# Optimization experiments

Hardware: AMD Instinct MI355X
Metric: run time of the kernel (lower is better)

The kernel has to match this reference:

```python
import jax, jax.numpy as jnp
import numpy as np

N_NODES = 100_000
N_FACES = 200_000
IN_CH = 128
OUT_CH = 29  # MLP out = OUT_CH + 3


def setup_inputs() -> dict:
    key = jax.random.key(0)
    k_pos, k_faces, k_ff, k_w1, k_w2 = jax.random.split(key, 5)
    pos = jax.random.normal(k_pos, (N_NODES, 3), dtype=jnp.float32)
    faces = jax.random.randint(k_faces, (N_FACES, 3), 0, N_NODES, dtype=jnp.int32)
    face_features = jax.random.normal(k_ff, (N_FACES, IN_CH), dtype=jnp.float32)
    d_in = IN_CH + 6
    W1 = jax.random.normal(k_w1, (d_in, IN_CH), dtype=jnp.float32) / np.sqrt(d_in)
    b1 = jnp.zeros((IN_CH,), dtype=jnp.float32)
    W2 = jax.random.normal(k_w2, (IN_CH, OUT_CH + 3), dtype=jnp.float32) / np.sqrt(IN_CH)
    b2 = jnp.zeros((OUT_CH + 3,), dtype=jnp.float32)
    return {"pos": pos, "face_features": face_features, "W1": W1, "b1": b1,
            "W2": W2, "b2": b2, "faces": faces}


def reference(pos, face_features, W1, b1, W2, b2, faces):
    def mlp(x):
        return jax.nn.relu(x @ W1 + b1) @ W2 + b2

    p0 = pos[faces[:, 0]]  # [F,3]
    p1 = pos[faces[:, 1]]
    p2 = pos[faces[:, 2]]

    g0 = mlp(jnp.concatenate([p1 - p0, p2 - p0, face_features], axis=1))
    g1 = mlp(jnp.concatenate([p2 - p1, p0 - p1, face_features], axis=1))
    g2 = mlp(jnp.concatenate([p0 - p2, p1 - p2, face_features], axis=1))

    face_features_out = (g0[:, 3:] + g1[:, 3:] + g2[:, 3:]) / 3.0  # [F,OUT_CH]

    # scatter_mean of per-corner deltas onto nodes; torch cat order matches
    # faces.T.flatten() = [faces[:,0], faces[:,1], faces[:,2]]
    vals = jnp.concatenate([g0[:, :3], g1[:, :3], g2[:, :3]], axis=0)  # [3F,3]
    idx = jnp.concatenate([faces[:, 0], faces[:, 1], faces[:, 2]], axis=0)  # [3F]
    sums = jax.ops.segment_sum(vals, idx, num_segments=N_NODES)
    counts = jax.ops.segment_sum(jnp.ones((vals.shape[0],), vals.dtype), idx,
                                 num_segments=N_NODES)
    delta_pos = sums / jnp.clip(counts, 1.0)[:, None]  # [N,3]

    new_pos = pos + delta_pos
    return (delta_pos, new_pos, face_features_out)
```

## Files before the change

### kernel.cpp

```cpp
#include <hip/hip_runtime.h>
#include <hip/hip_bf16.h>

#define N_NODES 100000
#define N_FACES 200000
#define FM 32
#define ROWS 96
#define XS 168
#define HS 136
#define WCS 40
#define W2S 136
#define NCH 5

typedef __attribute__((ext_vector_type(8))) short s8v;
typedef __attribute__((ext_vector_type(4))) short s4v;
typedef __attribute__((ext_vector_type(4))) float f4v;

static __device__ __forceinline__ short f2bf(float x) {
  __hip_bfloat16 h = __float2bfloat16(x);
  short s;
  __builtin_memcpy(&s, &h, 2);
  return s;
}

__global__ __launch_bounds__(256) void prep_kernel(
    const float* __restrict__ W1, const float* __restrict__ W2,
    short* __restrict__ w1t, short* __restrict__ w2t)
{
  int t = blockIdx.x * 256 + threadIdx.x;
  if (t < NCH * 128 * WCS) {
    int kc = t / (128 * WCS);
    int r = t % (128 * WCS);
    int n = r / WCS, kk = r % WCS;
    float v = 0.f;
    if (kk < 32) {
      int k = kc * 32 + kk;
      int gk = (k < 128) ? (k + 6) : (k < 134 ? k - 128 : -1);
      if (gk >= 0) v = W1[gk * 128 + n];
    }
    w1t[t] = f2bf(v);
  }
  if (t < 32 * W2S) {
    int o = t / W2S, k = t % W2S;
    float v = (k < 128) ? W2[k * 32 + o] : 0.f;
    w2t[t] = f2bf(v);
  }
}

__global__ __launch_bounds__(256) void face_kernel(
    const float* __restrict__ pos, const float* __restrict__ ffeat,
    const float* __restrict__ b1, const float* __restrict__ b2,
    const int* __restrict__ faces,
    const short* __restrict__ w1t_g, const short* __restrict__ w2t_g,
    float* __restrict__ out_ff, float* __restrict__ sums, int* __restrict__ cnt)
{
  __shared__ short xh[ROWS * XS];
  __shared__ short wb[2][128 * WCS];
  __shared__ short w2[32 * W2S];

  const int t = threadIdx.x;
  const int lane = t & 63;
  const int wv = t >> 6;
  const int l15 = lane & 15;
  const int lq = lane >> 4;
  const int kq = lq * 8;
  const int fbase = blockIdx.x * FM;

  {
    const unsigned* src = (const unsigned*)w2t_g;
    unsigned* dst = (unsigned*)w2;
#pragma unroll
    for (int i = 0; i < 9; ++i) {
      int idx = i * 256 + t;
      if (idx < (32 * W2S) / 2) dst[idx] = src[idx];
    }
  }
#pragma unroll
  for (int i = 0; i < 4; ++i) {
    int e = i * 256 + t;
    int floc = e >> 5, c4 = e & 31;
    f4v v = *(const f4v*)(ffeat + ((size_t)(fbase + floc) << 7) + (c4 << 2));
    s4v s;
    s.x = f2bf(v.x); s.y = f2bf(v.y); s.z = f2bf(v.z); s.w = f2bf(v.w);
    *(s4v*)&xh[(0 * FM + floc) * XS + (c4 << 2)] = s;
    *(s4v*)&xh[(1 * FM + floc) * XS + (c4 << 2)] = s;
    *(s4v*)&xh[(2 * FM + floc) * XS + (c4 << 2)] = s;
  }
  if (t < ROWS) {
    int v = t >> 5, floc = t & 31, face = fbase + floc;
    int vb = (v == 2) ? 0 : v + 1;
    int vc = (v == 0) ? 2 : v - 1;
    int ia = faces[face * 3 + v];
    int ib = faces[face * 3 + vb];
    int ic = faces[face * 3 + vc];
    float ax = pos[ia * 3 + 0], ay = pos[ia * 3 + 1], az = pos[ia * 3 + 2];
    float bx = pos[ib * 3 + 0], by = pos[ib * 3 + 1], bz = pos[ib * 3 + 2];
    float cx = pos[ic * 3 + 0], cy = pos[ic * 3 + 1], cz = pos[ic * 3 + 2];
    short* xr = &xh[t * XS];
    xr[128] = f2bf(bx - ax); xr[129] = f2bf(by - ay); xr[130] = f2bf(bz - az);
    xr[131] = f2bf(cx - ax); xr[132] = f2bf(cy - ay); xr[133] = f2bf(cz - az);
#pragma unroll
    for (int c = 134; c < XS; ++c) xr[c] = 0;
  }
  const unsigned* w1u = (const unsigned*)w1t_g;
  {
    unsigned* dst = (unsigned*)wb[0];
#pragma unroll
    for (int i = 0; i < 10; ++i) dst[i * 256 + t] = w1u[i * 256 + t];
  }
  __syncthreads();

  f4v acc[6][2];
#pragma unroll
  for (int m = 0; m < 6; ++m)
#pragma unroll
    for (int n = 0; n < 2; ++n) acc[m][n] = (f4v){0.f, 0.f, 0.f, 0.f};

#pragma unroll
  for (int kc = 0; kc < NCH; ++kc) {
    if (kc + 1 < NCH) {
      unsigned* dst = (unsigned*)wb[(kc + 1) & 1];
      const unsigned* src = w1u + (kc + 1) * (128 * WCS / 2);
#pragma unroll
      for (int i = 0; i < 10; ++i) dst[i * 256 + t] = src[i * 256 + t];
    }
    const short* wc = wb[kc & 1];
    s8v bf0 = *(const s8v*)&wc[((wv * 2 + 0) * 16 + l15) * WCS + kq];
    s8v bf1 = *(const s8v*)&wc[((wv * 2 + 1) * 16 + l15) * WCS + kq];
#pragma unroll
    for (int m = 0; m < 6; ++m) {
      s8v af = *(const s8v*)&xh[(m * 16 + l15) * XS + kc * 32 + kq];
      acc[m][0] = __builtin_amdgcn_mfma_f32_16x16x32_bf16(af, bf0, acc[m][0], 0, 0, 0);
      acc[m][1] = __builtin_amdgcn_mfma_f32_16x16x32_bf16(af, bf1, acc[m][1], 0, 0, 0);
    }
    __syncthreads();
  }

#pragma unroll
  for (int n = 0; n < 2; ++n) {
    int j = (wv * 2 + n) * 16 + l15;
    float bj = b1[j];
#pragma unroll
    for (int m = 0; m < 6; ++m) {
      int rb = m * 16 + lq * 4;
#pragma unroll
      for (int r = 0; r < 4; ++r) {
        float h = acc[m][n][r] + bj;
        xh[(rb + r) * HS + j] = f2bf(fmaxf(h, 0.f));
      }
    }
  }
  __syncthreads();

  f4v a2[3];
#pragma unroll
  for (int c = 0; c < 3; ++c) a2[c] = (f4v){0.f, 0.f, 0.f, 0.f};
  const int ct0 = wv * 3;
#pragma unroll
  for (int kk = 0; kk < 4; ++kk) {
    int kof = kk * 32 + kq;
#pragma unroll
    for (int c = 0; c < 3; ++c) {
      int ct = ct0 + c, mt = ct >> 1, n = ct & 1;
      s8v a = *(const s8v*)&xh[(mt * 16 + l15) * HS + kof];
      s8v b = *(const s8v*)&w2[(n * 16 + l15) * W2S + kof];
      a2[c] = __builtin_amdgcn_mfma_f32_16x16x32_bf16(a, b, a2[c], 0, 0, 0);
    }
  }
  __syncthreads();

  float* gsum = (float*)xh;
#pragma unroll
  for (int c = 0; c < 3; ++c) {
    int ct = ct0 + c, mt = ct >> 1, n = ct & 1;
    int o = n * 16 + l15;
    float bo = b2[o];
#pragma unroll
    for (int r = 0; r < 4; ++r) {
      int row = mt * 16 + lq * 4 + r;
      float g = a2[c][r] + bo;
      if (o < 3) {
        int v = row >> 5, floc = row & 31;
        int node = faces[(fbase + floc) * 3 + v];
        atomicAdd(&sums[node * 3 + o], g);
        if (o == 0) atomicAdd(&cnt[node], 1);
      } else {
        gsum[row * 29 + (o - 3)] = g;
      }
    }
  }
  __syncthreads();

#pragma unroll
  for (int i = 0; i < 4; ++i) {
    int e = i * 256 + t;
    if (e < FM * 29) {
      int floc = e / 29, c = e % 29;
      float s = gsum[floc * 29 + c] + gsum[(FM + floc) * 29 + c] + gsum[(2 * FM + floc) * 29 + c];
      out_ff[(size_t)(fbase + floc) * 29 + c] = s * (1.0f / 3.0f);
    }
  }
}

__global__ __launch_bounds__(256) void node_kernel(
    const float* __restrict__ pos, const float* __restrict__ sums,
    const int* __restrict__ cnt, float* __restrict__ out)
{
  int n = blockIdx.x * 256 + threadIdx.x;
  if (n >= N_NODES) return;
  float c = fmaxf((float)cnt[n], 1.0f);
#pragma unroll
  for (int o = 0; o < 3; ++o) {
    float d = sums[n * 3 + o] / c;
    out[n * 3 + o] = d;
    out[3 * N_NODES + n * 3 + o] = pos[n * 3 + o] + d;
  }
}

extern "C" void kernel_launch(void* const* d_in, const int* in_sizes, int n_in,
                              void* d_out, int out_size, void* d_ws, size_t ws_size,
                              hipStream_t stream) {
  const float* pos   = (const float*)d_in[0];
  const float* ffeat = (const float*)d_in[1];
  const float* W1    = (const float*)d_in[2];
  const float* b1    = (const float*)d_in[3];
  const float* W2    = (const float*)d_in[4];
  const float* b2    = (const float*)d_in[5];
  const int*   faces = (const int*)d_in[6];
  float* out = (float*)d_out;

  float* sums = (float*)d_ws;
  int*   cnt  = (int*)(sums + 3 * N_NODES);
  short* w1t  = (short*)(cnt + N_NODES);
  short* w2t  = w1t + NCH * 128 * WCS;

  hipMemsetAsync(d_ws, 0, (size_t)(3 * N_NODES + N_NODES) * 4, stream);
  prep_kernel<<<100, 256, 0, stream>>>(W1, W2, w1t, w2t);
  face_kernel<<<N_FACES / FM, 256, 0, stream>>>(pos, ffeat, b1, b2, faces, w1t, w2t,
                                                out + 6 * N_NODES, sums, cnt);
  node_kernel<<<(N_NODES + 255) / 256, 256, 0, stream>>>(pos, sums, cnt, out);
}
```

Before: 296.2 us.

## Make face kernel persistent with register-resident weights and double-buffered tile prefetch

The face kernel becomes a persistent grid of 512 blocks of 512 threads, each looping over many 32-face tiles. W1 and W2 fragments are held in registers, loaded once per block, instead of being streamed through shared memory for every tile. Face features, face indices and edge vectors for the next tile are prefetched into double-buffered shared memory while the current tile's MFMAs run. Features are stored once, not three times, and the per-corner outputs are summed with LDS atomics. The cost is more registers per thread, lower occupancy, and some repeated MFMAs on identical feature fragments.

```diff
diff --git a/kernel.cpp b/kernel.cpp
--- a/kernel.cpp
+++ b/kernel.cpp
@@ -5,11 +5,13 @@
 #define N_FACES 200000
 #define FM 32
 #define ROWS 96
-#define XS 168
+#define NTILES (N_FACES / FM)
+#define GRID 512
+#define FS 136
+#define ES 40
 #define HS 136
-#define WCS 40
-#define W2S 136
-#define NCH 5
+#define W1K 160
+#define W2K 128
 
 typedef __attribute__((ext_vector_type(8))) short s8v;
 typedef __attribute__((ext_vector_type(4))) short s4v;
@@ -27,35 +29,31 @@
     short* __restrict__ w1t, short* __restrict__ w2t)
 {
   int t = blockIdx.x * 256 + threadIdx.x;
-  if (t < NCH * 128 * WCS) {
-    int kc = t / (128 * WCS);
-    int r = t % (128 * WCS);
-    int n = r / WCS, kk = r % WCS;
+  if (t < 128 * W1K) {
+    int n = t / W1K, k = t % W1K;
     float v = 0.f;
-    if (kk < 32) {
-      int k = kc * 32 + kk;
-      int gk = (k < 128) ? (k + 6) : (k < 134 ? k - 128 : -1);
-      if (gk >= 0) v = W1[gk * 128 + n];
-    }
+    if (k < 128) v = W1[(k + 6) * 128 + n];
+    else if (k < 134) v = W1[(k - 128) * 128 + n];
     w1t[t] = f2bf(v);
   }
-  if (t < 32 * W2S) {
-    int o = t / W2S, k = t % W2S;
-    float v = (k < 128) ? W2[k * 32 + o] : 0.f;
-    w2t[t] = f2bf(v);
-  }
-}
-
-__global__ __launch_bounds__(256) void face_kernel(
+  if (t < 32 * W2K) {
+    int o = t / W2K, k = t % W2K;
+    w2t[t] = f2bf(W2[k * 32 + o]);
+  }
+}
+
+__global__ __launch_bounds__(512, 4) void face_kernel(
     const float* __restrict__ pos, const float* __restrict__ ffeat,
     const float* __restrict__ b1, const float* __restrict__ b2,
     const int* __restrict__ faces,
     const short* __restrict__ w1t_g, const short* __restrict__ w2t_g,
     float* __restrict__ out_ff, float* __restrict__ sums, int* __restrict__ cnt)
 {
-  __shared__ short xh[ROWS * XS];
-  __shared__ short wb[2][128 * WCS];
-  __shared__ short w2[32 * W2S];
+  __shared__ short xff[2][FM * FS];
+  __shared__ short xe[2][ROWS * ES];
+  __shared__ short hbuf[ROWS * HS];
+  __shared__ int   nidb[2][ROWS];
+  __shared__ float gsumb[FM * 30];
 
   const int t = threadIdx.x;
   const int lane = t & 63;
@@ -63,140 +61,172 @@
   const int l15 = lane & 15;
   const int lq = lane >> 4;
   const int kq = lq * 8;
-  const int fbase = blockIdx.x * FM;
+  const int nsel = wv & 1;
+
+  s8v bw1[5], bw2[4];
+#pragma unroll
+  for (int kc = 0; kc < 5; ++kc)
+    bw1[kc] = *(const s8v*)(w1t_g + (wv * 16 + l15) * W1K + kc * 32 + kq);
+#pragma unroll
+  for (int kk = 0; kk < 4; ++kk)
+    bw2[kk] = *(const s8v*)(w2t_g + (nsel * 16 + l15) * W2K + kk * 32 + kq);
+  const float b1j = b1[wv * 16 + l15];
+  const float b2o = b2[nsel * 16 + l15];
+
+  if (t < 2 * ROWS) {
+    int b = t / ROWS, row = t - b * ROWS;
+    s8v z = (s8v){0, 0, 0, 0, 0, 0, 0, 0};
+    *(unsigned*)&xe[b][row * ES + 6] = 0u;
+    *(s8v*)&xe[b][row * ES + 8] = z;
+    *(s8v*)&xe[b][row * ES + 16] = z;
+    *(s8v*)&xe[b][row * ES + 24] = z;
+    *(s8v*)&xe[b][row * ES + 32] = z;
+  }
 
   {
-    const unsigned* src = (const unsigned*)w2t_g;
-    unsigned* dst = (unsigned*)w2;
-#pragma unroll
-    for (int i = 0; i < 9; ++i) {
-      int idx = i * 256 + t;
-      if (idx < (32 * W2S) / 2) dst[idx] = src[idx];
-    }
-  }
-#pragma unroll
-  for (int i = 0; i < 4; ++i) {
-    int e = i * 256 + t;
-    int floc = e >> 5, c4 = e & 31;
-    f4v v = *(const f4v*)(ffeat + ((size_t)(fbase + floc) << 7) + (c4 << 2));
-    s4v s;
-    s.x = f2bf(v.x); s.y = f2bf(v.y); s.z = f2bf(v.z); s.w = f2bf(v.w);
-    *(s4v*)&xh[(0 * FM + floc) * XS + (c4 << 2)] = s;
-    *(s4v*)&xh[(1 * FM + floc) * XS + (c4 << 2)] = s;
-    *(s4v*)&xh[(2 * FM + floc) * XS + (c4 << 2)] = s;
-  }
-  if (t < ROWS) {
-    int v = t >> 5, floc = t & 31, face = fbase + floc;
-    int vb = (v == 2) ? 0 : v + 1;
-    int vc = (v == 0) ? 2 : v - 1;
-    int ia = faces[face * 3 + v];
-    int ib = faces[face * 3 + vb];
-    int ic = faces[face * 3 + vc];
-    float ax = pos[ia * 3 + 0], ay = pos[ia * 3 + 1], az = pos[ia * 3 + 2];
-    float bx = pos[ib * 3 + 0], by = pos[ib * 3 + 1], bz = pos[ib * 3 + 2];
-    float cx = pos[ic * 3 + 0], cy = pos[ic * 3 + 1], cz = pos[ic * 3 + 2];
-    short* xr = &xh[t * XS];
-    xr[128] = f2bf(bx - ax); xr[129] = f2bf(by - ay); xr[130] = f2bf(bz - az);
-    xr[131] = f2bf(cx - ax); xr[132] = f2bf(cy - ay); xr[133] = f2bf(cz - az);
-#pragma unroll
-    for (int c = 134; c < XS; ++c) xr[c] = 0;
-  }
-  const unsigned* w1u = (const unsigned*)w1t_g;
-  {
-    unsigned* dst = (unsigned*)wb[0];
-#pragma unroll
-    for (int i = 0; i < 10; ++i) dst[i * 256 + t] = w1u[i * 256 + t];
+    int fb = blockIdx.x * FM;
+    const float* fp = ffeat + ((size_t)(fb + (t >> 4)) << 7) + ((t & 15) << 3);
+    f4v v0 = *(const f4v*)fp, v1 = *(const f4v*)(fp + 4);
+    s8v s;
+    s[0] = f2bf(v0.x); s[1] = f2bf(v0.y); s[2] = f2bf(v0.z); s[3] = f2bf(v0.w);
+    s[4] = f2bf(v1.x); s[5] = f2bf(v1.y); s[6] = f2bf(v1.z); s[7] = f2bf(v1.w);
+    *(s8v*)&xff[0][(t >> 4) * FS + ((t & 15) << 3)] = s;
+    int rt = t - 384;
+    if ((unsigned)rt < 96u) {
+      int face = fb + (rt & 31), v = rt >> 5;
+      int i0 = faces[face * 3 + 0], i1 = faces[face * 3 + 1], i2 = faces[face * 3 + 2];
+      int ia = (v == 0) ? i0 : ((v == 1) ? i1 : i2);
+      int ib = (v == 0) ? i1 : ((v == 1) ? i2 : i0);
+      int ic = (v == 0) ? i2 : ((v == 1) ? i0 : i1);
+      float ax = pos[ia * 3], ay = pos[ia * 3 + 1], az = pos[ia * 3 + 2];
+      float bx = pos[ib * 3], by = pos[ib * 3 + 1], bz = pos[ib * 3 + 2];
+      float cx = pos[ic * 3], cy = pos[ic * 3 + 1], cz = pos[ic * 3 + 2];
+      s4v e;
+      e[0] = f2bf(bx - ax); e[1] = f2bf(by - ay); e[2] = f2bf(bz - az); e[3] = f2bf(cx - ax);
+      *(s4v*)&xe[0][rt * ES] = e;
+      unsigned p2 = (unsigned)(unsigned short)f2bf(cy - ay) |
+                    ((unsigned)(unsigned short)f2bf(cz - az) << 16);
+      *(unsigned*)&xe[0][rt * ES + 4] = p2;
+      nidb[0][rt] = ia;
+    }
   }
   __syncthreads();
 
-  f4v acc[6][2];
-#pragma unroll
-  for (int m = 0; m < 6; ++m)
-#pragma unroll
-    for (int n = 0; n < 2; ++n) acc[m][n] = (f4v){0.f, 0.f, 0.f, 0.f};
-
-#pragma unroll
-  for (int kc = 0; kc < NCH; ++kc) {
-    if (kc + 1 < NCH) {
-      unsigned* dst = (unsigned*)wb[(kc + 1) & 1];
-      const unsigned* src = w1u + (kc + 1) * (128 * WCS / 2);
-#pragma unroll
-      for (int i = 0; i < 10; ++i) dst[i * 256 + t] = src[i * 256 + t];
-    }
-    const short* wc = wb[kc & 1];
-    s8v bf0 = *(const s8v*)&wc[((wv * 2 + 0) * 16 + l15) * WCS + kq];
-    s8v bf1 = *(const s8v*)&wc[((wv * 2 + 1) * 16 + l15) * WCS + kq];
+  int iter = 0;
+  for (int tile = blockIdx.x; tile < NTILES; tile += GRID, ++iter) {
+    const int cur = iter & 1, nxt = cur ^ 1;
+    const int fb_c = tile * FM;
+    const int tile_n = tile + GRID;
+    const bool hn = tile_n < NTILES;
+    const int fb_n = tile_n * FM;
+    const int rt = t - 384;
+
+    f4v nv0, nv1;
+    int ni0 = 0, ni1 = 0, ni2 = 0;
+    if (hn) {
+      const float* fp = ffeat + ((size_t)(fb_n + (t >> 4)) << 7) + ((t & 15) << 3);
+      nv0 = *(const f4v*)fp;
+      nv1 = *(const f4v*)(fp + 4);
+      if ((unsigned)rt < 96u) {
+        int face = fb_n + (rt & 31);
+        ni0 = faces[face * 3 + 0]; ni1 = faces[face * 3 + 1]; ni2 = faces[face * 3 + 2];
+      }
+    }
+
+    f4v acc1[6];
+#pragma unroll
+    for (int m = 0; m < 6; ++m) acc1[m] = (f4v){0.f, 0.f, 0.f, 0.f};
+    const short* xf = &xff[cur][0];
+    const short* xeb = &xe[cur][0];
+#pragma unroll
+    for (int kc = 0; kc < 4; ++kc) {
+      s8v a0 = *(const s8v*)&xf[l15 * FS + kc * 32 + kq];
+      s8v a1 = *(const s8v*)&xf[(16 + l15) * FS + kc * 32 + kq];
+      acc1[0] = __builtin_amdgcn_mfma_f32_16x16x32_bf16(a0, bw1[kc], acc1[0], 0, 0, 0);
+      acc1[1] = __builtin_amdgcn_mfma_f32_16x16x32_bf16(a1, bw1[kc], acc1[1], 0, 0, 0);
+      acc1[2] = __builtin_amdgcn_mfma_f32_16x16x32_bf16(a0, bw1[kc], acc1[2], 0, 0, 0);
+      acc1[3] = __builtin_amdgcn_mfma_f32_16x16x32_bf16(a1, bw1[kc], acc1[3], 0, 0, 0);
+      acc1[4] = __builtin_amdgcn_mfma_f32_16x16x32_bf16(a0, bw1[kc], acc1[4], 0, 0, 0);
+      acc1[5] = __builtin_amdgcn_mfma_f32_16x16x32_bf16(a1, bw1[kc], acc1[5], 0, 0, 0);
+    }
 #pragma unroll
     for (int m = 0; m < 6; ++m) {
-      s8v af = *(const s8v*)&xh[(m * 16 + l15) * XS + kc * 32 + kq];
-      acc[m][0] = __builtin_amdgcn_mfma_f32_16x16x32_bf16(af, bf0, acc[m][0], 0, 0, 0);
-      acc[m][1] = __builtin_amdgcn_mfma_f32_16x16x32_bf16(af, bf1, acc[m][1], 0, 0, 0);
-    }
+      s8v a = *(const s8v*)&xeb[(m * 16 + l15) * ES + kq];
+      acc1[m] = __builtin_amdgcn_mfma_f32_16x16x32_bf16(a, bw1[4], acc1[m], 0, 0, 0);
+    }
+
     __syncthreads();
-  }
-
-#pragma unroll
-  for (int n = 0; n < 2; ++n) {
-    int j = (wv * 2 + n) * 16 + l15;
-    float bj = b1[j];
-#pragma unroll
-    for (int m = 0; m < 6; ++m) {
-      int rb = m * 16 + lq * 4;
-#pragma unroll
-      for (int r = 0; r < 4; ++r) {
-        float h = acc[m][n][r] + bj;
-        xh[(rb + r) * HS + j] = f2bf(fmaxf(h, 0.f));
+
+    {
+      int j = wv * 16 + l15;
+#pragma unroll
+      for (int m = 0; m < 6; ++m)
+#pragma unroll
+        for (int r = 0; r < 4; ++r)
+          hbuf[(m * 16 + lq * 4 + r) * HS + j] = f2bf(fmaxf(acc1[m][r] + b1j, 0.f));
+    }
+    for (int e = t; e < FM * 30; e += 512) gsumb[e] = 0.f;
+
+    float pax = 0, pay = 0, paz = 0, pbx = 0, pby = 0, pbz = 0, pcx = 0, pcy = 0, pcz = 0;
+    int ia_s = 0, ib_s = 0, ic_s = 0;
+    if (hn) {
+      s8v s;
+      s[0] = f2bf(nv0.x); s[1] = f2bf(nv0.y); s[2] = f2bf(nv0.z); s[3] = f2bf(nv0.w);
+      s[4] = f2bf(nv1.x); s[5] = f2bf(nv1.y); s[6] = f2bf(nv1.z); s[7] = f2bf(nv1.w);
+      *(s8v*)&xff[nxt][(t >> 4) * FS + ((t & 15) << 3)] = s;
+      if ((unsigned)rt < 96u) {
+        int v = rt >> 5;
+        ia_s = (v == 0) ? ni0 : ((v == 1) ? ni1 : ni2);
+        ib_s = (v == 0) ? ni1 : ((v == 1) ? ni2 : ni0);
+        ic_s = (v == 0) ? ni2 : ((v == 1) ? ni0 : ni1);
+        pax = pos[ia_s * 3]; pay = pos[ia_s * 3 + 1]; paz = pos[ia_s * 3 + 2];
+        pbx = pos[ib_s * 3]; pby = pos[ib_s * 3 + 1]; pbz = pos[ib_s * 3 + 2];
+        pcx = pos[ic_s * 3]; pcy = pos[ic_s * 3 + 1]; pcz = pos[ic_s * 3 + 2];
       }
     }
-  }
-  __syncthreads();
-
-  f4v a2[3];
-#pragma unroll
-  for (int c = 0; c < 3; ++c) a2[c] = (f4v){0.f, 0.f, 0.f, 0.f};
-  const int ct0 = wv * 3;
-#pragma unroll
-  for (int kk = 0; kk < 4; ++kk) {
-    int kof = kk * 32 + kq;
-#pragma unroll
-    for (int c = 0; c < 3; ++c) {
-      int ct = ct0 + c, mt = ct >> 1, n = ct & 1;
-      s8v a = *(const s8v*)&xh[(mt * 16 + l15) * HS + kof];
-      s8v b = *(const s8v*)&w2[(n * 16 + l15) * W2S + kof];
-      a2[c] = __builtin_amdgcn_mfma_f32_16x16x32_bf16(a, b, a2[c], 0, 0, 0);
-    }
-  }
-  __syncthreads();
-
-  float* gsum = (float*)xh;
-#pragma unroll
-  for (int c = 0; c < 3; ++c) {
-    int ct = ct0 + c, mt = ct >> 1, n = ct & 1;
-    int o = n * 16 + l15;
-    float bo = b2[o];
-#pragma unroll
-    for (int r = 0; r < 4; ++r) {
-      int row = mt * 16 + lq * 4 + r;
-      float g = a2[c][r] + bo;
-      if (o < 3) {
-        int v = row >> 5, floc = row & 31;
-        int node = faces[(fbase + floc) * 3 + v];
-        atomicAdd(&sums[node * 3 + o], g);
-        if (o == 0) atomicAdd(&cnt[node], 1);
-      } else {
-        gsum[row * 29 + (o - 3)] = g;
+    __syncthreads();
+
+#pragma unroll
+    for (int p = 0; p < 2; ++p) {
+      if (p == 0 || wv < 4) {
+        int m = (wv >> 1) + p * 4;
+        f4v c2 = (f4v){0.f, 0.f, 0.f, 0.f};
+#pragma unroll
+        for (int kk = 0; kk < 4; ++kk) {
+          s8v a = *(const s8v*)&hbuf[(m * 16 + l15) * HS + kk * 32 + kq];
+          c2 = __builtin_amdgcn_mfma_f32_16x16x32_bf16(a, bw2[kk], c2, 0, 0, 0);
+        }
+        int o = nsel * 16 + l15;
+#pragma unroll
+        for (int r = 0; r < 4; ++r) {
+          int row = m * 16 + lq * 4 + r;
+          float g = c2[r] + b2o;
+          if (o < 3) {
+            int node = nidb[cur][row];
+            atomicAdd(&sums[node * 3 + o], g);
+            if (o == 0) atomicAdd(&cnt[node], 1);
+          } else {
+            atomicAdd(&gsumb[(row & 31) * 30 + (o - 3)], g);
+          }
+        }
       }
     }
-  }
-  __syncthreads();
-
-#pragma unroll
-  for (int i = 0; i < 4; ++i) {
-    int e = i * 256 + t;
-    if (e < FM * 29) {
-      int floc = e / 29, c = e % 29;
-      float s = gsum[floc * 29 + c] + gsum[(FM + floc) * 29 + c] + gsum[(2 * FM + floc) * 29 + c];
-      out_ff[(size_t)(fbase + floc) * 29 + c] = s * (1.0f / 3.0f);
+
+    if (hn && (unsigned)rt < 96u) {
+      s4v e;
+      e[0] = f2bf(pbx - pax); e[1] = f2bf(pby - pay);
+      e[2] = f2bf(pbz - paz); e[3] = f2bf(pcx - pax);
+      *(s4v*)&xe[nxt][rt * ES] = e;
+      unsigned p2 = (unsigned)(unsigned short)f2bf(pcy - pay) |
+                    ((unsigned)(unsigned short)f2bf(pcz - paz) << 16);
+      *(unsigned*)&xe[nxt][rt * ES + 4] = p2;
+      nidb[nxt][rt] = ia_s;
+    }
+    __syncthreads();
+
+    for (int e = t; e < FM * 29; e += 512) {
+      int floc = e / 29, c = e - floc * 29;
+      out_ff[((size_t)(fb_c + floc)) * 29 + c] = gsumb[floc * 30 + c] * (1.0f / 3.0f);
     }
   }
 }
@@ -231,11 +261,11 @@
   float* sums = (float*)d_ws;
   int*   cnt  = (int*)(sums + 3 * N_NODES);
   short* w1t  = (short*)(cnt + N_NODES);
-  short* w2t  = w1t + NCH * 128 * WCS;
+  short* w2t  = w1t + 128 * W1K;
 
   hipMemsetAsync(d_ws, 0, (size_t)(3 * N_NODES + N_NODES) * 4, stream);
-  prep_kernel<<<100, 256, 0, stream>>>(W1, W2, w1t, w2t);
-  face_kernel<<<N_FACES / FM, 256, 0, stream>>>(pos, ffeat, b1, b2, faces, w1t, w2t,
-                                                out + 6 * N_NODES, sums, cnt);
+  prep_kernel<<<80, 256, 0, stream>>>(W1, W2, w1t, w2t);
+  face_kernel<<<GRID, 512, 0, stream>>>(pos, ffeat, b1, b2, faces, w1t, w2t,
+                                        out + 6 * N_NODES, sums, cnt);
   node_kernel<<<(N_NODES + 255) / 256, 256, 0, stream>>>(pos, sums, cnt, out);
 }
```

New measurement: 264.1 us. -10.8%, faster.
